# Kernel optimization log

Measured on AMD Instinct MI355X. Metric: run time of the kernel, lower is better.

Reference implementation:

```python
import jax, jax.numpy as jnp
import numpy as np

B, N, L = 32, 128, 1024
DRUG_DIM, TGT_DIM, HID, H = 256, 1280, 512, 8
HD = HID // H  # 64
NEG = jnp.float32(-1e9)


def setup_inputs() -> dict:
    key = jax.random.key(0)
    ks = jax.random.split(key, 9)
    drug_nodes = jax.random.normal(ks[0], (B, N, DRUG_DIM), dtype=jnp.float32)
    target_seq = jax.random.normal(ks[1], (B, L, TGT_DIM), dtype=jnp.float32)
    # masks: random valid lengths in [max//2, max], True = valid
    dlen = jax.random.randint(ks[2], (B,), N // 2, N + 1)
    tlen = jax.random.randint(ks[3], (B,), L // 2, L + 1)
    drug_mask = jnp.arange(N)[None, :] < dlen[:, None]
    target_mask = jnp.arange(L)[None, :] < tlen[:, None]
    # params (nn.Linear default init ~ U(-1/sqrt(fan_in), ...); randn*0.02 ok for a reference)
    Wd = jax.random.normal(ks[4], (DRUG_DIM, HID), dtype=jnp.float32) / np.sqrt(DRUG_DIM)
    bd = jnp.zeros((HID,), dtype=jnp.float32)
    Wt = jax.random.normal(ks[5], (TGT_DIM, HID), dtype=jnp.float32) / np.sqrt(TGT_DIM)
    bt = jnp.zeros((HID,), dtype=jnp.float32)
    Wb = jax.random.normal(ks[6], (H, HD, HD), dtype=jnp.float32) * 0.02
    return {"drug_nodes": drug_nodes, "drug_mask": drug_mask,
            "target_seq": target_seq, "target_mask": target_mask,
            "Wd": Wd, "bd": bd, "Wt": Wt, "bt": bt, "Wb": Wb}


def reference(drug_nodes, drug_mask, target_seq, target_mask, Wd, bd, Wt, bt, Wb):
    # project and split heads -> (h, B, n, hd) / (h, B, l, hd)
    d = drug_nodes @ Wd + bd                                  # (B, N, HID)
    t = target_seq @ Wt + bt                                  # (B, L, HID)
    dh = d.reshape(B, N, H, HD).transpose(2, 0, 1, 3)         # (H, B, N, HD)
    th = t.reshape(B, L, H, HD).transpose(2, 0, 1, 3)         # (H, B, L, HD)

    dW = jnp.einsum('hbnd,hde->hbne', dh, Wb)                 # bilinear map
    attn = jnp.einsum('hbne,hble->hbnl', dW, th)              # (H, B, N, L)

    mask = (drug_mask[:, :, None] & target_mask[:, None, :])[None]  # (1, B, N, L)
    scores = jnp.where(mask, attn, NEG)

    # drug-side softmax over protein residues (axis=-1), dropout is identity (eval)
    attn_d = jnp.where(mask, jax.nn.softmax(scores, axis=-1), 0.0)
    ctx_d = jnp.einsum('hbnl,hble->hbne', attn_d, th)         # (H, B, N, HD)
    dmf = drug_mask[None, :, :, None].astype(ctx_d.dtype)
    ctx_d = (ctx_d * dmf).sum(axis=2) / jnp.clip(dmf.sum(axis=2), 1.0)  # (H, B, HD)
    ctx_d = ctx_d.transpose(1, 0, 2).reshape(B, -1)           # (B, HID)

    # target-side softmax over atoms (axis=-2)
    attn_t = jnp.where(mask, jax.nn.softmax(scores, axis=-2), 0.0)
    ctx_t = jnp.einsum('hbnl,hbne->hble', attn_t, dh)         # (H, B, L, HD)
    tmf = target_mask[None, :, :, None].astype(ctx_t.dtype)
    ctx_t = (ctx_t * tmf).sum(axis=2) / jnp.clip(tmf.sum(axis=2), 1.0)  # (H, B, HD)
    ctx_t = ctx_t.transpose(1, 0, 2).reshape(B, -1)           # (B, HID)

    return jnp.concatenate([ctx_d, ctx_t], axis=-1)           # (B, 2*HID)
```

## Files before the change

kernel.cpp:

```cpp
#include <hip/hip_runtime.h>
#include <hip/hip_bf16.h>
#include <math.h>

#define B_ 32
#define N_ 128
#define L_ 1024
#define DD_ 256
#define TD_ 1280
#define HID_ 512
#define H_ 8
#define HD_ 64

#define WS_D    0
#define WS_RM   (WS_D   + 2097152)
#define WS_RIZ  (WS_RM  + 32768)
#define WS_RMT  (WS_RIZ + 32768)
#define WS_RZT  (WS_RMT + 524288)
#define WS_RWT  (WS_RZT + 524288)
#define WS_CNT  (WS_RWT + 524288)
#define WS_WT   (WS_CNT + 64)
#define WS_THB  (WS_WT  + 327680)
#define WS_DWB  (WS_THB + 8388608)
#define WS_ABF  (WS_DWB + 1048576)

using bf16x8 = __attribute__((ext_vector_type(8))) short;
using floatx4 = __attribute__((ext_vector_type(4))) float;

static __device__ __forceinline__ unsigned short f2bf(float f) {
  unsigned int u = __float_as_uint(f);
  unsigned int r = (u + 0x7FFFu + ((u >> 16) & 1u)) >> 16;
  return (unsigned short)r;
}
static __device__ __forceinline__ float bf2f(unsigned short s) {
  return __uint_as_float(((unsigned int)s) << 16);
}
static __device__ __forceinline__ void gload16(const void* g, void* l) {
  __builtin_amdgcn_global_load_lds(
      (const __attribute__((address_space(1))) void*)g,
      (__attribute__((address_space(3))) void*)l, 16, 0, 0);
}

__global__ __launch_bounds__(256) void count_kernel(const int* __restrict__ dmask,
                                                    const int* __restrict__ tmask,
                                                    int* __restrict__ cnts) {
  __shared__ int red[256];
  const int b = blockIdx.x, tid = threadIdx.x;
  const bool dint = (dmask[0] == 1);
  const bool tint = (tmask[0] == 1);
  int s = 0;
  if (dint) {
    for (int i = tid; i < N_; i += 256) s += (dmask[(size_t)b*N_ + i] != 0);
  } else {
    const unsigned char* p = (const unsigned char*)dmask;
    for (int i = tid; i < N_; i += 256) s += (p[(size_t)b*N_ + i] != 0);
  }
  red[tid] = s; __syncthreads();
  for (int off = 128; off > 0; off >>= 1) { if (tid < off) red[tid] += red[tid+off]; __syncthreads(); }
  if (tid == 0) cnts[b*2] = red[0];
  __syncthreads();
  s = 0;
  if (tint) {
    for (int i = tid; i < L_; i += 256) s += (tmask[(size_t)b*L_ + i] != 0);
  } else {
    const unsigned char* p = (const unsigned char*)tmask;
    for (int i = tid; i < L_; i += 256) s += (p[(size_t)b*L_ + i] != 0);
  }
  red[tid] = s; __syncthreads();
  for (int off = 128; off > 0; off >>= 1) { if (tid < off) red[tid] += red[tid+off]; __syncthreads(); }
  if (tid == 0) cnts[b*2+1] = red[0];
}

__global__ __launch_bounds__(256) void a2bf_kernel(const float* __restrict__ A,
                                                   unsigned short* __restrict__ Abf,
                                                   long n) {
  long i = ((long)blockIdx.x * 256 + threadIdx.x) * 8;
  const long stride = (long)gridDim.x * 256 * 8;
  for (; i < n; i += stride) {
    float4 x = *(const float4*)(A + i);
    float4 y = *(const float4*)(A + i + 4);
    union { unsigned short s[8]; uint4 u; } p;
    p.s[0] = f2bf(x.x); p.s[1] = f2bf(x.y); p.s[2] = f2bf(x.z); p.s[3] = f2bf(x.w);
    p.s[4] = f2bf(y.x); p.s[5] = f2bf(y.y); p.s[6] = f2bf(y.z); p.s[7] = f2bf(y.w);
    *(uint4*)(Abf + i) = p.u;
  }
}

__global__ __launch_bounds__(256) void transpose_bf16_kernel(
    const float* __restrict__ W, unsigned short* __restrict__ WT, int K, int Nd) {
  __shared__ float tile[32][33];
  const int tid = threadIdx.x;
  const int n0 = blockIdx.x * 32, k0 = blockIdx.y * 32;
  const int c = tid & 31, r0 = tid >> 5;
#pragma unroll
  for (int i = 0; i < 4; i++) {
    const int r = r0 + i * 8;
    tile[c][r] = W[(size_t)(k0 + r) * Nd + n0 + c];
  }
  __syncthreads();
#pragma unroll
  for (int i = 0; i < 4; i++) {
    const int r = r0 + i * 8;
    WT[(size_t)(n0 + r) * K + k0 + c] = f2bf(tile[r][c]);
  }
}

__global__ __launch_bounds__(256) void gemm_t_mfma_kernel(
    const unsigned short* __restrict__ Abf, const unsigned short* __restrict__ WT,
    const float* __restrict__ bias, unsigned short* __restrict__ thb, int K) {
  __shared__ __align__(16) unsigned short As[8192];
  __shared__ __align__(16) unsigned short Bs[8192];
  const int tid = threadIdx.x;
  const int lin = blockIdx.x;
  const int xcd = lin & 7, sq = lin >> 3;
  const int n_t = sq & 3, m_t = (sq >> 2) + xcd * 32;
  const int m0 = m_t * 128, n0 = n_t * 128;
  const int lane = tid & 63, wave = tid >> 6;
  const int wm = wave & 1, wn = wave >> 1;
  const int quad = lane >> 4, lrow = lane & 15;

  floatx4 acc[4][4];
#pragma unroll
  for (int i = 0; i < 4; i++)
#pragma unroll
    for (int j = 0; j < 4; j++) acc[i][j] = (floatx4){0.f, 0.f, 0.f, 0.f};

  int srcoff[2][2];
#pragma unroll
  for (int call = 0; call < 2; call++) {
    const int i = call * 256 + tid;
    const int r = i >> 2;
    const int c = (i & 3) ^ ((r >> 1) & 3);
#pragma unroll
    for (int g = 0; g < 2; g++) srcoff[call][g] = r * K + g * 32 + c * 8;
  }
  const unsigned short* Abase = Abf + (size_t)m0 * K;
  const unsigned short* Bbase = WT + (size_t)n0 * K;

  for (int k0 = 0; k0 < K; k0 += 64) {
    __syncthreads();
#pragma unroll
    for (int g = 0; g < 2; g++) {
#pragma unroll
      for (int call = 0; call < 2; call++) {
        const int dst = g * 4096 + (call * 256 + wave * 64) * 8;
        gload16(Abase + k0 + srcoff[call][g], &As[dst]);
        gload16(Bbase + k0 + srcoff[call][g], &Bs[dst]);
      }
    }
    __syncthreads();
#pragma unroll
    for (int g = 0; g < 2; g++) {
      bf16x8 bfr[4];
#pragma unroll
      for (int j = 0; j < 4; j++) {
        const int br = wn * 64 + j * 16 + lrow;
        bfr[j] = *(const bf16x8*)&Bs[g * 4096 + (br * 4 + (quad ^ ((br >> 1) & 3))) * 8];
      }
#pragma unroll
      for (int i = 0; i < 4; i++) {
        const int ar = wm * 64 + i * 16 + lrow;
        bf16x8 afr = *(const bf16x8*)&As[g * 4096 + (ar * 4 + (quad ^ ((ar >> 1) & 3))) * 8];
#pragma unroll
        for (int j = 0; j < 4; j++)
          acc[i][j] = __builtin_amdgcn_mfma_f32_16x16x32_bf16(afr, bfr[j], acc[i][j], 0, 0, 0);
      }
    }
  }

  float bj[4];
#pragma unroll
  for (int j = 0; j < 4; j++) bj[j] = bias[n0 + wn * 64 + j * 16 + lrow];
#pragma unroll
  for (int i = 0; i < 4; i++) {
#pragma unroll
    for (int j = 0; j < 4; j++) {
      const int gcol = n0 + wn * 64 + j * 16 + lrow;
      const int hh = gcol >> 6, e = gcol & 63;
#pragma unroll
      for (int r = 0; r < 4; r++) {
        const int grow = m0 + wm * 64 + i * 16 + quad * 4 + r;
        const int bb = grow >> 10, l = grow & 1023;
        thb[(((size_t)bb * H_ + hh) * L_ + l) * HD_ + e] = f2bf(acc[i][j][r] + bj[j]);
      }
    }
  }
}

__global__ __launch_bounds__(256) void gemm_bias_kernel(
    const float* __restrict__ A, const float* __restrict__ W,
    const float* __restrict__ bias, float* __restrict__ C,
    int M, int K, int Nd) {
  __shared__ float As[8][132];
  __shared__ float Bs[8][132];
  const int tid = threadIdx.x;
  const int m0 = blockIdx.y * 128, n0 = blockIdx.x * 128;
  const int lr = tid >> 1, lc = (tid & 1) * 4;
  const int wr = tid >> 5, wc = (tid & 31) * 4;
  const int tm = (tid >> 4) * 4, tn = (tid & 15) * 4;

  float acc[2][2][4][4];
#pragma unroll
  for (int a = 0; a < 2; a++)
#pragma unroll
    for (int bq = 0; bq < 2; bq++)
#pragma unroll
      for (int i = 0; i < 4; i++)
#pragma unroll
        for (int j = 0; j < 4; j++) acc[a][bq][i][j] = 0.f;

  const float* Aptr = A + (size_t)(m0 + lr) * K + lc;
  const float* Wptr = W + (size_t)wr * Nd + n0 + wc;

  for (int k0 = 0; k0 < K; k0 += 8) {
    float4 a4 = *(const float4*)(Aptr + k0);
    float4 w4 = *(const float4*)(Wptr + (size_t)k0 * Nd);
    __syncthreads();
    As[lc+0][lr] = a4.x; As[lc+1][lr] = a4.y; As[lc+2][lr] = a4.z; As[lc+3][lr] = a4.w;
    *(float4*)&Bs[wr][wc] = w4;
    __syncthreads();
#pragma unroll
    for (int kk = 0; kk < 8; kk++) {
      float4 a0 = *(const float4*)&As[kk][tm];
      float4 a1 = *(const float4*)&As[kk][tm + 64];
      float4 b0 = *(const float4*)&Bs[kk][tn];
      float4 b1 = *(const float4*)&Bs[kk][tn + 64];
      const float av0[4] = {a0.x, a0.y, a0.z, a0.w};
      const float av1[4] = {a1.x, a1.y, a1.z, a1.w};
      const float bv0[4] = {b0.x, b0.y, b0.z, b0.w};
      const float bv1[4] = {b1.x, b1.y, b1.z, b1.w};
#pragma unroll
      for (int i = 0; i < 4; i++)
#pragma unroll
        for (int j = 0; j < 4; j++) {
          acc[0][0][i][j] += av0[i] * bv0[j];
          acc[0][1][i][j] += av0[i] * bv1[j];
          acc[1][0][i][j] += av1[i] * bv0[j];
          acc[1][1][i][j] += av1[i] * bv1[j];
        }
    }
  }
  float4 bias0 = *(const float4*)&bias[n0 + tn];
  float4 bias1 = *(const float4*)&bias[n0 + tn + 64];
  const float bb0[4] = {bias0.x, bias0.y, bias0.z, bias0.w};
  const float bb1[4] = {bias1.x, bias1.y, bias1.z, bias1.w};
#pragma unroll
  for (int mh = 0; mh < 2; mh++)
#pragma unroll
    for (int i = 0; i < 4; i++) {
      const int row = m0 + mh * 64 + tm + i;
      float* cp = C + (size_t)row * Nd + n0;
      float4 o0, o1;
      o0.x = acc[mh][0][i][0] + bb0[0]; o0.y = acc[mh][0][i][1] + bb0[1];
      o0.z = acc[mh][0][i][2] + bb0[2]; o0.w = acc[mh][0][i][3] + bb0[3];
      o1.x = acc[mh][1][i][0] + bb1[0]; o1.y = acc[mh][1][i][1] + bb1[1];
      o1.z = acc[mh][1][i][2] + bb1[2]; o1.w = acc[mh][1][i][3] + bb1[3];
      *(float4*)(cp + tn) = o0;
      *(float4*)(cp + tn + 64) = o1;
    }
}

__global__ __launch_bounds__(256) void dw_kernel(
    const float* __restrict__ dproj, const float* __restrict__ Wb,
    unsigned short* __restrict__ dWb) {
  __shared__ float wb_s[64 * 64];
  const int tid = threadIdx.x;
  const int hb = blockIdx.x, b = hb >> 3, h = hb & 7;
  for (int i = tid; i < 4096; i += 256) wb_s[i] = Wb[(size_t)h * 4096 + i];
  __syncthreads();
  const int n = tid >> 1, half = tid & 1;
  float acc[32];
#pragma unroll
  for (int e = 0; e < 32; e++) acc[e] = 0.f;
  const float* dpr = dproj + ((size_t)(b * N_ + n)) * HID_ + h * HD_;
  for (int k = 0; k < 64; k++) {
    const float a = dpr[k];
    const float* wr = &wb_s[k * 64 + half * 32];
#pragma unroll
    for (int e = 0; e < 32; e++) acc[e] += a * wr[e];
  }
  unsigned short* outp = dWb + ((size_t)hb * N_ + n) * HD_ + half * 32;
#pragma unroll
  for (int e = 0; e < 32; e++) outp[e] = f2bf(acc[e]);
}

__device__ __forceinline__ void mfma_S_tile(
    const unsigned short* __restrict__ thp, const unsigned short* __restrict__ dwp,
    float* __restrict__ S_s, int ncnt, int lv, int tid) {
  const int lane = tid & 63, wave = tid >> 6;
  const int quad = lane >> 4, lr = lane & 15;
  const int noff = (wave & 1) * 64, loff = (wave >> 1) * 32;

  floatx4 acc[4][2];
#pragma unroll
  for (int i = 0; i < 4; i++)
#pragma unroll
    for (int j = 0; j < 2; j++) acc[i][j] = (floatx4){0.f, 0.f, 0.f, 0.f};

#pragma unroll
  for (int kc = 0; kc < 2; kc++) {
    bf16x8 bfr[2];
#pragma unroll
    for (int j = 0; j < 2; j++)
      bfr[j] = *(const bf16x8*)&thp[(size_t)(loff + j * 16 + lr) * HD_ + kc * 32 + quad * 8];
#pragma unroll
    for (int i = 0; i < 4; i++) {
      bf16x8 afr = *(const bf16x8*)&dwp[(size_t)(noff + i * 16 + lr) * HD_ + kc * 32 + quad * 8];
#pragma unroll
      for (int j = 0; j < 2; j++)
        acc[i][j] = __builtin_amdgcn_mfma_f32_16x16x32_bf16(afr, bfr[j], acc[i][j], 0, 0, 0);
    }
  }
#pragma unroll
  for (int i = 0; i < 4; i++)
#pragma unroll
    for (int j = 0; j < 2; j++)
#pragma unroll
      for (int r = 0; r < 4; r++) {
        const int n = noff + i * 16 + quad * 4 + r;
        const int li = loff + j * 16 + lr;
        const bool ok = (n < ncnt) && (li < lv);
        S_s[n * 69 + li] = ok ? acc[i][j][r] : -1e9f;
      }
}

__global__ __launch_bounds__(256, 4) void attn_stats_kernel(
    const unsigned short* __restrict__ thb, const unsigned short* __restrict__ dWb,
    const int* __restrict__ cnts, float* __restrict__ rwt,
    float* __restrict__ rmt, float* __restrict__ rzt) {
  __shared__ float S_s[128 * 69];
  __shared__ float red[256];
  __shared__ float zb_s[256], wb_s[256];
  __shared__ float cm_s[64], ics_s[64];
  const int tid = threadIdx.x;
  const int hb = blockIdx.x >> 4, lt = blockIdx.x & 15;
  const int b = hb >> 3;
  const int ncnt = cnts[b * 2], lcnt = cnts[b * 2 + 1];
  const int l0g = lt * 64;
  if (l0g >= lcnt) return;
  const int lv = min(64, lcnt - l0g);

  mfma_S_tile(thb + ((size_t)hb * L_ + l0g) * HD_, dWb + (size_t)hb * N_ * HD_,
              S_s, ncnt, lv, tid);
  __syncthreads();

  {
    const int l = tid & 63, q = tid >> 6;
    float pm = -INFINITY;
    for (int n = q * 32; n < q * 32 + 32; n++) pm = fmaxf(pm, S_s[n * 69 + l]);
    red[tid] = pm;
  }
  __syncthreads();
  if (tid < 64)
    cm_s[tid] = fmaxf(fmaxf(red[tid], red[tid + 64]), fmaxf(red[tid + 128], red[tid + 192]));
  __syncthreads();
  {
    const int l = tid & 63, q = tid >> 6;
    const float cm = cm_s[l];
    float ps = 0.f;
    for (int n = q * 32; n < q * 32 + 32; n++) ps += __expf(S_s[n * 69 + l] - cm);
    red[tid] = ps;
  }
  __syncthreads();
  if (tid < 64)
    ics_s[tid] = 1.f / (red[tid] + red[tid + 64] + red[tid + 128] + red[tid + 192]);
  __syncthreads();
  {
    const int n = tid & 127, half = tid >> 7;
    const float* Sr = &S_s[n * 69];
    const int lb = half * 32, le = min(lb + 32, lv);
    float tmax = -INFINITY;
    for (int l = lb; l < le; l++) tmax = fmaxf(tmax, Sr[l]);
    red[tid] = tmax;
    __syncthreads();
    const float tm = fmaxf(red[n], red[n + 128]);
    float z = 0.f, w = 0.f;
    for (int l = lb; l < le; l++) {
      const float s = Sr[l];
      z += __expf(s - tm);
      w += __expf(s - cm_s[l]) * ics_s[l];
    }
    zb_s[tid] = z; wb_s[tid] = w;
    __syncthreads();
    if (tid < 128) {
      const size_t o = ((size_t)hb * 16 + lt) * 128 + tid;
      rmt[o] = tm;
      rzt[o] = zb_s[tid] + zb_s[tid + 128];
      rwt[o] = wb_s[tid] + wb_s[tid + 128];
    }
  }
}

__global__ __launch_bounds__(256) void attn_combine_kernel(
    const float* __restrict__ rmt, const float* __restrict__ rzt,
    const float* __restrict__ rwt, const float* __restrict__ dproj,
    const int* __restrict__ cnts, float* __restrict__ rm_g,
    float* __restrict__ riz_g, float* __restrict__ outp) {
  __shared__ float red[256];
  __shared__ float w_s[128];
  const int tid = threadIdx.x;
  const int hb = blockIdx.x, b = hb >> 3, h = hb & 7;
  const int ncnt = cnts[b * 2], lcnt = cnts[b * 2 + 1];
  const int ntl = (lcnt + 63) >> 6;
  if (tid < 128) {
    const int n = tid;
    float m = -INFINITY;
    for (int t = 0; t < ntl; t++)
      m = fmaxf(m, rmt[((size_t)hb * 16 + t) * 128 + n]);
    float Z = 0.f, w = 0.f;
    for (int t = 0; t < ntl; t++) {
      const size_t o = ((size_t)hb * 16 + t) * 128 + n;
      Z += rzt[o] * __expf(rmt[o] - m);
      w += rwt[o];
    }
    rm_g[hb * 128 + n] = m;
    riz_g[hb * 128 + n] = (n < ncnt) ? 1.f / Z : 0.f;
    w_s[n] = (n < ncnt) ? w : 0.f;
  }
  __syncthreads();
  const int e = tid & 63, q = tid >> 6;
  float p = 0.f;
  const int nb = q * 32, ne = min(nb + 32, ncnt);
  for (int n = nb; n < ne; n++)
    p += w_s[n] * dproj[((size_t)(b * N_ + n)) * HID_ + h * HD_ + e];
  red[tid] = p;
  __syncthreads();
  if (tid < 64) {
    const float s = red[tid] + red[tid + 64] + red[tid + 128] + red[tid + 192];
    outp[(size_t)b * (2 * HID_) + HID_ + h * HD_ + tid] = s / (float)lcnt;
  }
}

__global__ __launch_bounds__(256, 4) void attn_v_kernel(
    const unsigned short* __restrict__ thb, const unsigned short* __restrict__ dWb,
    const int* __restrict__ cnts, const float* __restrict__ rm_g,
    const float* __restrict__ riz_g, float* __restrict__ outp) {
  __shared__ float S_s[128 * 69];
  __shared__ float red[256];
  __shared__ float rm_s[128], riz_s[128], v_s[64];
  const int tid = threadIdx.x;
  const int hb = blockIdx.x >> 4, lt = blockIdx.x & 15;
  const int b = hb >> 3, h = hb & 7;
  const int ncnt = cnts[b * 2], lcnt = cnts[b * 2 + 1];
  const int l0g = lt * 64;
  if (l0g >= lcnt) return;
  const int lv = min(64, lcnt - l0g);

  if (tid < 128) {
    rm_s[tid] = rm_g[hb * 128 + tid];
    riz_s[tid] = riz_g[hb * 128 + tid];
  }
  const unsigned short* thp = thb + ((size_t)hb * L_ + l0g) * HD_;
  mfma_S_tile(thp, dWb + (size_t)hb * N_ * HD_, S_s, ncnt, lv, tid);
  __syncthreads();

  {
    const int l = tid & 63, q = tid >> 6;
    float vp = 0.f;
    for (int n = q * 32; n < q * 32 + 32; n++)
      vp += __expf(S_s[n * 69 + l] - rm_s[n]) * riz_s[n];
    red[tid] = vp;
  }
  __syncthreads();
  const float incnt = 1.f / (float)ncnt;
  if (tid < 64) {
    const float v = (tid < lv)
        ? (red[tid] + red[tid + 64] + red[tid + 128] + red[tid + 192]) * incnt
        : 0.f;
    v_s[tid] = v;
  }
  __syncthreads();
  {
    const int e = tid & 63, q = tid >> 6;
    float p = 0.f;
    for (int l = q * 16; l < q * 16 + 16; l++)
      p += v_s[l] * bf2f(thp[(size_t)l * HD_ + e]);
    red[tid] = p;
  }
  __syncthreads();
  if (tid < 64) {
    const float s = red[tid] + red[tid + 64] + red[tid + 128] + red[tid + 192];
    if (s != 0.f)
      atomicAdd(&outp[(size_t)b * (2 * HID_) + h * HD_ + tid], s);
  }
}

extern "C" void kernel_launch(void* const* d_in, const int* in_sizes, int n_in,
                              void* d_out, int out_size, void* d_ws, size_t ws_size,
                              hipStream_t stream) {
  const float* drug = (const float*)d_in[0];
  const int* dmask = (const int*)d_in[1];
  const float* tseq = (const float*)d_in[2];
  const int* tmask = (const int*)d_in[3];
  const float* Wd = (const float*)d_in[4];
  const float* bd = (const float*)d_in[5];
  const float* Wt = (const float*)d_in[6];
  const float* bt = (const float*)d_in[7];
  const float* Wb = (const float*)d_in[8];
  float* out = (float*)d_out;
  float* ws = (float*)d_ws;

  float* dp = ws + WS_D;
  float* rm = ws + WS_RM;
  float* riz = ws + WS_RIZ;
  float* rmt = ws + WS_RMT;
  float* rzt = ws + WS_RZT;
  float* rwt = ws + WS_RWT;
  int* cnts = (int*)(ws + WS_CNT);
  unsigned short* wtT = (unsigned short*)(ws + WS_WT);
  unsigned short* thb = (unsigned short*)(ws + WS_THB);
  unsigned short* dWb = (unsigned short*)(ws + WS_DWB);
  unsigned short* abf = (unsigned short*)(ws + WS_ABF);

  count_kernel<<<B_, 256, 0, stream>>>(dmask, tmask, cnts);
  hipMemsetAsync(out, 0, (size_t)out_size * sizeof(float), stream);
  a2bf_kernel<<<1024, 256, 0, stream>>>(tseq, abf, (long)B_ * L_ * TD_);
  transpose_bf16_kernel<<<dim3(HID_ / 32, TD_ / 32), 256, 0, stream>>>(Wt, wtT, TD_, HID_);
  gemm_t_mfma_kernel<<<(HID_ / 128) * ((B_ * L_) / 128), 256, 0, stream>>>(
      abf, wtT, bt, thb, TD_);
  gemm_bias_kernel<<<dim3(HID_ / 128, (B_ * N_) / 128), 256, 0, stream>>>(
      drug, Wd, bd, dp, B_ * N_, DD_, HID_);
  dw_kernel<<<B_ * H_, 256, 0, stream>>>(dp, Wb, dWb);
  attn_stats_kernel<<<B_ * H_ * 16, 256, 0, stream>>>(thb, dWb, cnts, rwt, rmt, rzt);
  attn_combine_kernel<<<B_ * H_, 256, 0, stream>>>(rmt, rzt, rwt, dp, cnts, rm, riz, out);
  attn_v_kernel<<<B_ * H_ * 16, 256, 0, stream>>>(thb, dWb, cnts, rm, riz, out);
}
```

Baseline: 471.9 us.

## Fuse fp32-to-bf16 conversion of target sequence into the projection GEMM

Removes the standalone conversion kernel and its bf16 workspace. The target projection GEMM now loads fp32 rows into registers, converts them to bf16 and writes them to swizzled LDS. It also double-buffers the weight tile and prefetches the next k-step to overlap loads with MFMA work. This avoids a full write and re-read of an intermediate bf16 copy. In exchange, each block reads twice as many bytes of the activation, which is reused across the four column tiles, and register pressure rises.

```diff
diff --git a/kernel.cpp b/kernel.cpp
--- a/kernel.cpp
+++ b/kernel.cpp
@@ -21,7 +21,6 @@
 #define WS_WT   (WS_CNT + 64)
 #define WS_THB  (WS_WT  + 327680)
 #define WS_DWB  (WS_THB + 8388608)
-#define WS_ABF  (WS_DWB + 1048576)
 
 using bf16x8 = __attribute__((ext_vector_type(8))) short;
 using floatx4 = __attribute__((ext_vector_type(4))) float;
@@ -70,21 +69,6 @@
   if (tid == 0) cnts[b*2+1] = red[0];
 }
 
-__global__ __launch_bounds__(256) void a2bf_kernel(const float* __restrict__ A,
-                                                   unsigned short* __restrict__ Abf,
-                                                   long n) {
-  long i = ((long)blockIdx.x * 256 + threadIdx.x) * 8;
-  const long stride = (long)gridDim.x * 256 * 8;
-  for (; i < n; i += stride) {
-    float4 x = *(const float4*)(A + i);
-    float4 y = *(const float4*)(A + i + 4);
-    union { unsigned short s[8]; uint4 u; } p;
-    p.s[0] = f2bf(x.x); p.s[1] = f2bf(x.y); p.s[2] = f2bf(x.z); p.s[3] = f2bf(x.w);
-    p.s[4] = f2bf(y.x); p.s[5] = f2bf(y.y); p.s[6] = f2bf(y.z); p.s[7] = f2bf(y.w);
-    *(uint4*)(Abf + i) = p.u;
-  }
-}
-
 __global__ __launch_bounds__(256) void transpose_bf16_kernel(
     const float* __restrict__ W, unsigned short* __restrict__ WT, int K, int Nd) {
   __shared__ float tile[32][33];
@@ -104,11 +88,11 @@
   }
 }
 
-__global__ __launch_bounds__(256) void gemm_t_mfma_kernel(
-    const unsigned short* __restrict__ Abf, const unsigned short* __restrict__ WT,
+__global__ __launch_bounds__(256, 3) void gemm_t_mfma_kernel(
+    const float* __restrict__ A, const unsigned short* __restrict__ WT,
     const float* __restrict__ bias, unsigned short* __restrict__ thb, int K) {
   __shared__ __align__(16) unsigned short As[8192];
-  __shared__ __align__(16) unsigned short Bs[8192];
+  __shared__ __align__(16) unsigned short Bs[2][8192];
   const int tid = threadIdx.x;
   const int lin = blockIdx.x;
   const int xcd = lin & 7, sq = lin >> 3;
@@ -133,28 +117,71 @@
 #pragma unroll
     for (int g = 0; g < 2; g++) srcoff[call][g] = r * K + g * 32 + c * 8;
   }
-  const unsigned short* Abase = Abf + (size_t)m0 * K;
+
+  const int ar_ = tid >> 2;
+  const int kc_ = (tid & 3) * 16;
+  const int g_  = kc_ >> 5;
+  const int cq0 = (kc_ & 31) >> 3;
+
+  const float* Abase = A + (size_t)m0 * K;
   const unsigned short* Bbase = WT + (size_t)n0 * K;
 
-  for (int k0 = 0; k0 < K; k0 += 64) {
-    __syncthreads();
-#pragma unroll
-    for (int g = 0; g < 2; g++) {
+  float4 apf[2][4];
+
+  auto aload = [&](int k0) {
+#pragma unroll
+    for (int i = 0; i < 2; i++) {
+      const float* src = Abase + (size_t)(ar_ + i * 64) * K + k0 + kc_;
+#pragma unroll
+      for (int j = 0; j < 4; j++) apf[i][j] = *(const float4*)(src + j * 4);
+    }
+  };
+  auto awrite = [&]() {
+#pragma unroll
+    for (int i = 0; i < 2; i++) {
+      const int r = ar_ + i * 64;
+      const int sw = (r >> 1) & 3;
+      union { unsigned short s[16]; bf16x8 v[2]; } p;
+#pragma unroll
+      for (int j = 0; j < 4; j++) {
+        p.s[j * 4 + 0] = f2bf(apf[i][j].x);
+        p.s[j * 4 + 1] = f2bf(apf[i][j].y);
+        p.s[j * 4 + 2] = f2bf(apf[i][j].z);
+        p.s[j * 4 + 3] = f2bf(apf[i][j].w);
+      }
+      *(bf16x8*)&As[g_ * 4096 + (r * 4 + ((cq0 + 0) ^ sw)) * 8] = p.v[0];
+      *(bf16x8*)&As[g_ * 4096 + (r * 4 + ((cq0 + 1) ^ sw)) * 8] = p.v[1];
+    }
+  };
+  auto bstage = [&](int buf, int k0) {
+#pragma unroll
+    for (int g = 0; g < 2; g++)
 #pragma unroll
       for (int call = 0; call < 2; call++) {
         const int dst = g * 4096 + (call * 256 + wave * 64) * 8;
-        gload16(Abase + k0 + srcoff[call][g], &As[dst]);
-        gload16(Bbase + k0 + srcoff[call][g], &Bs[dst]);
+        gload16(Bbase + k0 + srcoff[call][g], &Bs[buf][dst]);
       }
-    }
+  };
+
+  const int nkt = K / 64;
+  bstage(0, 0);
+  aload(0);
+
+  for (int t = 0; t < nkt; t++) {
+    awrite();
     __syncthreads();
+    if (t + 1 < nkt) {
+      bstage((t + 1) & 1, (t + 1) * 64);
+      aload((t + 1) * 64);
+    }
+    const unsigned short* Bp = Bs[t & 1];
 #pragma unroll
     for (int g = 0; g < 2; g++) {
       bf16x8 bfr[4];
 #pragma unroll
       for (int j = 0; j < 4; j++) {
         const int br = wn * 64 + j * 16 + lrow;
-        bfr[j] = *(const bf16x8*)&Bs[g * 4096 + (br * 4 + (quad ^ ((br >> 1) & 3))) * 8];
+        bfr[j] = *(const bf16x8*)&Bp[g * 4096 + (br * 4 + (quad ^ ((br >> 1) & 3))) * 8];
       }
 #pragma unroll
       for (int i = 0; i < 4; i++) {
@@ -165,6 +192,7 @@
           acc[i][j] = __builtin_amdgcn_mfma_f32_16x16x32_bf16(afr, bfr[j], acc[i][j], 0, 0, 0);
       }
     }
+    __syncthreads();
   }
 
   float bj[4];
@@ -509,14 +537,12 @@
   unsigned short* wtT = (unsigned short*)(ws + WS_WT);
   unsigned short* thb = (unsigned short*)(ws + WS_THB);
   unsigned short* dWb = (unsigned short*)(ws + WS_DWB);
-  unsigned short* abf = (unsigned short*)(ws + WS_ABF);
 
   count_kernel<<<B_, 256, 0, stream>>>(dmask, tmask, cnts);
   hipMemsetAsync(out, 0, (size_t)out_size * sizeof(float), stream);
-  a2bf_kernel<<<1024, 256, 0, stream>>>(tseq, abf, (long)B_ * L_ * TD_);
   transpose_bf16_kernel<<<dim3(HID_ / 32, TD_ / 32), 256, 0, stream>>>(Wt, wtT, TD_, HID_);
   gemm_t_mfma_kernel<<<(HID_ / 128) * ((B_ * L_) / 128), 256, 0, stream>>>(
-      abf, wtT, bt, thb, TD_);
+      tseq, wtT, bt, thb, TD_);
   gemm_bias_kernel<<<dim3(HID_ / 128, (B_ * N_) / 128), 256, 0, stream>>>(
       drug, Wd, bd, dp, B_ * N_, DD_, HID_);
   dw_kernel<<<B_ * H_, 256, 0, stream>>>(dp, Wb, dWb);
```

New measurement: 485.0 us. 1.03x slower.
